# Kernel tuning notes

Hardware: AMD Instinct MI355X
Metric: run time of the kernel (lower is better)

The kernel has to match this reference:

```python
import jax, jax.numpy as jnp
import numpy as np

B, IN, H, OUT = 8192, 1024, 1024, 512


def setup_inputs() -> dict:
    key = jax.random.key(0)
    ks = jax.random.split(key, 13)
    s_in = 1.0 / np.sqrt(IN + H)
    s_h = 1.0 / np.sqrt(H)
    return {
        "x": jax.random.normal(ks[0], (B, IN), jnp.float32),
        "h": jax.random.normal(ks[1], (B, H), jnp.float32),
        "c": jax.random.normal(ks[2], (B, H), jnp.float32),
        "Wi": jax.random.normal(ks[3], (IN + H, H), jnp.float32) * s_in,
        "bi": jax.random.normal(ks[4], (H,), jnp.float32) * s_in,
        "Wf": jax.random.normal(ks[5], (IN + H, H), jnp.float32) * s_in,
        "bf": jax.random.normal(ks[6], (H,), jnp.float32) * s_in,
        "Wo": jax.random.normal(ks[7], (IN + H, H), jnp.float32) * s_in,
        "bo": jax.random.normal(ks[8], (H,), jnp.float32) * s_in,
        "Wc": jax.random.normal(ks[9], (IN + H, H), jnp.float32) * s_in,
        "bc": jax.random.normal(ks[10], (H,), jnp.float32) * s_in,
        "Wy": jax.random.normal(ks[11], (H, OUT), jnp.float32) * s_h,
        "by": jax.random.normal(ks[12], (OUT,), jnp.float32) * s_h,
    }


def reference(x, h, c, Wi, bi, Wf, bf, Wo, bo, Wc, bc, Wy, by):
    # combined: [B, IN+H]
    combined = jnp.concatenate([x, h], axis=1)
    # Fuse the four gate matmuls into one [B, IN+H] x [IN+H, 4H] GEMM.
    W_all = jnp.concatenate([Wi, Wf, Wo, Wc], axis=1)        # [IN+H, 4H]
    b_all = jnp.concatenate([bi, bf, bo, bc], axis=0)        # [4H]
    gates = combined @ W_all + b_all                          # [B, 4H]
    gi, gf, go, gc = jnp.split(gates, 4, axis=1)
    i_t = jax.nn.sigmoid(gi)
    f_t = jax.nn.sigmoid(gf)
    o_t = jax.nn.sigmoid(go)
    c_tilde = jnp.tanh(gc)
    c_new = f_t * c + i_t * c_tilde
    h_new = o_t * jnp.tanh(c_new)
    y_hat = h_new @ Wy + by                                   # [B, OUT]
    return (y_hat, (h_new, c_new))
```

## Files before the change

kernel.cpp:

```cpp
#include <hip/hip_runtime.h>
#include <hip/hip_bf16.h>
#include <stdint.h>

#define B_ 8192
#define IN_ 1024
#define H_ 1024
#define OUT_ 512
#define KC 2048
#define N4 4096

typedef __bf16 bf16_t;
typedef __bf16 bf16x8 __attribute__((ext_vector_type(8)));
typedef float f32x4 __attribute__((ext_vector_type(4)));

__device__ __forceinline__ void gload_lds16(const void* g, void* l) {
  __builtin_amdgcn_global_load_lds(
      (const __attribute__((address_space(1))) uint32_t*)g,
      (__attribute__((address_space(3))) uint32_t*)l, 16, 0, 0);
}

__device__ __forceinline__ float fsigmoid(float x) {
  return __builtin_amdgcn_rcpf(1.0f + __expf(-x));
}
__device__ __forceinline__ float ftanh(float x) {
  return 2.0f * __builtin_amdgcn_rcpf(1.0f + __expf(-2.0f * x)) - 1.0f;
}


__global__ __launch_bounds__(256) void pack_combined(
    const float* __restrict__ x, const float* __restrict__ h,
    bf16_t* __restrict__ out) {
  const int row = blockIdx.x;
  const int j = threadIdx.x * 8;
  const float* src = (j < IN_) ? (x + (size_t)row * IN_ + j)
                               : (h + (size_t)row * H_ + (j - IN_));
  float4 a = ((const float4*)src)[0];
  float4 b = ((const float4*)src)[1];
  bf16x8 v;
  v[0] = (bf16_t)a.x; v[1] = (bf16_t)a.y; v[2] = (bf16_t)a.z; v[3] = (bf16_t)a.w;
  v[4] = (bf16_t)b.x; v[5] = (bf16_t)b.y; v[6] = (bf16_t)b.z; v[7] = (bf16_t)b.w;
  *(bf16x8*)(out + (size_t)row * KC + j) = v;
}

__global__ __launch_bounds__(256) void transpose_pack4(
    const float* __restrict__ Wi, const float* __restrict__ Wf,
    const float* __restrict__ Wo, const float* __restrict__ Wc,
    bf16_t* __restrict__ dst) {
  const int g = blockIdx.z;
  const float* src = (g == 0) ? Wi : (g == 1) ? Wf : (g == 2) ? Wo : Wc;
  __shared__ float tile[64][65];
  const int k0 = blockIdx.y * 64, n0 = blockIdx.x * 64;
  const int t = threadIdx.x;
  const int tr = t >> 4, tc4 = (t & 15) * 4;
#pragma unroll
  for (int r = 0; r < 4; ++r) {
    const int k = tr + r * 16;
    float4 v = *(const float4*)(src + (size_t)(k0 + k) * H_ + n0 + tc4);
    tile[k][tc4] = v.x; tile[k][tc4 + 1] = v.y;
    tile[k][tc4 + 2] = v.z; tile[k][tc4 + 3] = v.w;
  }
  __syncthreads();
  const int nr = t >> 3, kc8 = (t & 7) * 8;
#pragma unroll
  for (int r = 0; r < 2; ++r) {
    const int n = nr + r * 32;
    bf16x8 v;
#pragma unroll
    for (int q = 0; q < 8; ++q) v[q] = (bf16_t)tile[kc8 + q][n];
    *(bf16x8*)(dst + (size_t)((n0 + n) * 4 + g) * KC + k0 + kc8) = v;
  }
}

__global__ __launch_bounds__(256) void transpose_pack(
    const float* __restrict__ src, bf16_t* __restrict__ dst, int K, int N) {
  __shared__ float tile[64][65];
  const int k0 = blockIdx.y * 64, n0 = blockIdx.x * 64;
  const int t = threadIdx.x;
  const int tr = t >> 4, tc4 = (t & 15) * 4;
#pragma unroll
  for (int r = 0; r < 4; ++r) {
    const int k = tr + r * 16;
    float4 v = *(const float4*)(src + (size_t)(k0 + k) * N + n0 + tc4);
    tile[k][tc4] = v.x; tile[k][tc4 + 1] = v.y;
    tile[k][tc4 + 2] = v.z; tile[k][tc4 + 3] = v.w;
  }
  __syncthreads();
  const int nr = t >> 3, kc8 = (t & 7) * 8;
#pragma unroll
  for (int r = 0; r < 2; ++r) {
    const int n = nr + r * 32;
    bf16x8 v;
#pragma unroll
    for (int q = 0; q < 8; ++q) v[q] = (bf16_t)tile[kc8 + q][n];
    *(bf16x8*)(dst + (size_t)(n0 + n) * K + k0 + kc8) = v;
  }
}

__global__ __launch_bounds__(512) void gemm1_8ph(
    const bf16_t* __restrict__ A, const bf16_t* __restrict__ Bt,
    const float* __restrict__ c_in,
    const float* __restrict__ bi, const float* __restrict__ bfg,
    const float* __restrict__ bo, const float* __restrict__ bc,
    float* __restrict__ h_out, float* __restrict__ c_out,
    bf16_t* __restrict__ hb) {
  constexpr int K = KC;
  constexpr int NT = K / 64;
  __shared__ char lds[131072];

  const int tid = threadIdx.x;
  const int lane = tid & 63;
  const int w = tid >> 6;
  const int wr = w >> 2, wc = w & 3;
  const int l15 = lane & 15, l4 = lane >> 4;

  const int wg = blockIdx.x;
  const int swz = (wg & 7) * 64 + (wg >> 3);
  const int bx = swz >> 5;
  const int by = swz & 31;
  const int m0 = by * 256, n0 = bx * 256;

  const int jrow = lane >> 2;
  const int jcol = ((lane & 3) * 16) ^ ((lane >> 5) << 5);
  const char* Asrc = (const char*)A + (size_t)(m0 + w * 16 + jrow) * (K * 2) + jcol;
  const char* Bsrc = (const char*)Bt + (size_t)(n0 + w * 16 + jrow) * (K * 2) + jcol;
  char* ldsA = lds;
  char* ldsB = lds + 32768;
  const int wchunk = w * 2048;

#define STG_A(buf, h, tt) do {                                            \
    gload_lds16(Asrc + (size_t)(h) * 128 * (K * 2) + (size_t)(tt) * 128,  \
                ldsA + (buf) * 65536 + (h) * 16384 + wchunk);             \
    gload_lds16(Asrc + (size_t)(h) * 128 * (K * 2) + (size_t)(tt) * 128 + 64, \
                ldsA + (buf) * 65536 + (h) * 16384 + wchunk + 1024);      \
  } while (0)
#define STG_B(buf, h, tt) do {                                            \
    gload_lds16(Bsrc + (size_t)(h) * 128 * (K * 2) + (size_t)(tt) * 128,  \
                ldsB + (buf) * 65536 + (h) * 16384 + wchunk);             \
    gload_lds16(Bsrc + (size_t)(h) * 128 * (K * 2) + (size_t)(tt) * 128 + 64, \
                ldsB + (buf) * 65536 + (h) * 16384 + wchunk + 1024);      \
  } while (0)

  const int rdoff = l15 * 64 + ((l4 * 16) ^ ((l15 >> 3) << 5));
  const char* ldsArd = lds + wr * 16384 + rdoff;
  const char* ldsBrd = lds + 32768 + (wc >> 1) * 16384 + (wc & 1) * 8192 + rdoff;

  f32x4 acc[8][4] = {};
  bf16x8 falo[4][2], fahi[4][2], fb[4][2];

  STG_B(0, 0, 0); STG_B(0, 1, 0); STG_A(0, 0, 0); STG_A(0, 1, 0);
  asm volatile("s_waitcnt vmcnt(0)" ::: "memory");
  __builtin_amdgcn_s_barrier();

  for (int t = 0; t < NT; ++t) {
    const int buf = t & 1;
    const int nbuf = buf ^ 1;
    const char* ard = ldsArd + buf * 65536;
    const char* brd = ldsBrd + buf * 65536;
    const bool st1 = (t + 1 < NT);

#pragma unroll
    for (int mi = 0; mi < 2; ++mi)
#pragma unroll
      for (int kk = 0; kk < 2; ++kk)
        falo[mi][kk] = *(const bf16x8*)(ard + mi * 2048 + kk * 1024);
#pragma unroll
    for (int ni = 0; ni < 2; ++ni)
#pragma unroll
      for (int kk = 0; kk < 2; ++kk)
        fb[ni][kk] = *(const bf16x8*)(brd + ni * 2048 + kk * 1024);

    if (st1) {
      STG_B(nbuf, 0, t + 1); STG_B(nbuf, 1, t + 1);
      STG_A(nbuf, 0, t + 1); STG_A(nbuf, 1, t + 1);
    }

#pragma unroll
    for (int mi = 2; mi < 4; ++mi)
#pragma unroll
      for (int kk = 0; kk < 2; ++kk)
        falo[mi][kk] = *(const bf16x8*)(ard + mi * 2048 + kk * 1024);
#pragma unroll
    for (int ni = 2; ni < 4; ++ni)
#pragma unroll
      for (int kk = 0; kk < 2; ++kk)
        fb[ni][kk] = *(const bf16x8*)(brd + ni * 2048 + kk * 1024);

#pragma unroll
    for (int mi = 0; mi < 4; ++mi)
#pragma unroll
      for (int kk = 0; kk < 2; ++kk)
        fahi[mi][kk] = *(const bf16x8*)(ard + (mi + 4) * 2048 + kk * 1024);

    __builtin_amdgcn_s_setprio(1);
#pragma unroll
    for (int kk = 0; kk < 2; ++kk)
#pragma unroll
      for (int mi = 0; mi < 2; ++mi)
#pragma unroll
        for (int ni = 0; ni < 2; ++ni)
          acc[mi][ni] = __builtin_amdgcn_mfma_f32_16x16x32_bf16(
              falo[mi][kk], fb[ni][kk], acc[mi][ni], 0, 0, 0);

#pragma unroll
    for (int kk = 0; kk < 2; ++kk) {
#pragma unroll
      for (int mi = 0; mi < 2; ++mi)
#pragma unroll
        for (int ni = 2; ni < 4; ++ni)
          acc[mi][ni] = __builtin_amdgcn_mfma_f32_16x16x32_bf16(
              falo[mi][kk], fb[ni][kk], acc[mi][ni], 0, 0, 0);
#pragma unroll
      for (int mi = 2; mi < 4; ++mi)
#pragma unroll
        for (int ni = 0; ni < 2; ++ni)
          acc[mi][ni] = __builtin_amdgcn_mfma_f32_16x16x32_bf16(
              falo[mi][kk], fb[ni][kk], acc[mi][ni], 0, 0, 0);
    }

#pragma unroll
    for (int kk = 0; kk < 2; ++kk)
#pragma unroll
      for (int mi = 2; mi < 4; ++mi)
#pragma unroll
        for (int ni = 2; ni < 4; ++ni)
          acc[mi][ni] = __builtin_amdgcn_mfma_f32_16x16x32_bf16(
              falo[mi][kk], fb[ni][kk], acc[mi][ni], 0, 0, 0);

#pragma unroll
    for (int kk = 0; kk < 2; ++kk)
#pragma unroll
      for (int mi = 0; mi < 4; ++mi)
#pragma unroll
        for (int ni = 0; ni < 4; ++ni)
          acc[mi + 4][ni] = __builtin_amdgcn_mfma_f32_16x16x32_bf16(
              fahi[mi][kk], fb[ni][kk], acc[mi + 4][ni], 0, 0, 0);
    __builtin_amdgcn_s_setprio(0);

    if (st1) asm volatile("s_waitcnt vmcnt(0)" ::: "memory");
    __builtin_amdgcn_s_barrier();
  }

  const int hc0 = n0 >> 2;
  const int ehc = tid & 63;
  const int err0 = (tid >> 6) * 8;
  const float bI = bi[hc0 + ehc];
  const float bF = bfg[hc0 + ehc];
  const float bO = bo[hc0 + ehc];
  const float bC = bc[hc0 + ehc];

  for (int p = 0; p < 2; ++p) {
    __builtin_amdgcn_s_barrier();
    {
      float* dst = (float*)(lds + wr * 65536);
      const int mib = p * 4;
#pragma unroll
      for (int mi = 0; mi < 4; ++mi)
#pragma unroll
        for (int ni = 0; ni < 4; ++ni) {
          const int col = wc * 64 + ni * 16 + l15;
          const int hc = col >> 2, g = col & 3;
#pragma unroll
          for (int q = 0; q < 4; ++q) {
            const int rr = mi * 16 + l4 * 4 + q;
            dst[rr * 256 + ((hc ^ rr) * 4) + g] = acc[mib + mi][ni][q];
          }
        }
    }
    __builtin_amdgcn_s_barrier();
#pragma unroll
    for (int half = 0; half < 2; ++half) {
      const float* src = (const float*)(lds + half * 65536);
#pragma unroll
      for (int r = 0; r < 8; ++r) {
        const int rr = err0 + r;
        f32x4 gq = *(const f32x4*)&src[rr * 256 + ((ehc ^ rr) * 4)];
        const size_t gidx =
            (size_t)(m0 + half * 128 + p * 64 + rr) * H_ + hc0 + ehc;
        float I = fsigmoid(gq[0] + bI);
        float F = fsigmoid(gq[1] + bF);
        float O = fsigmoid(gq[2] + bO);
        float Ct = ftanh(gq[3] + bC);
        float cn = F * c_in[gidx] + I * Ct;
        float hn = O * ftanh(cn);
        c_out[gidx] = cn;
        h_out[gidx] = hn;
        hb[gidx] = (bf16_t)hn;
      }
    }
  }
#undef STG_A
#undef STG_B
}

__global__ __launch_bounds__(256) void gemm_bt_f32(
    const bf16_t* __restrict__ A, const bf16_t* __restrict__ Bt,
    float* __restrict__ Cout, const float* __restrict__ bias,
    int M, int N, int K) {
  __shared__ bf16_t As[128 * 64];
  __shared__ bf16_t Bs[128 * 64];
  const int tid = threadIdx.x;
  const int lane = tid & 63;
  const int wave = tid >> 6;
  const int m0 = blockIdx.y * 128;
  const int n0 = blockIdx.x * 128;
  const int wr = wave >> 1, wc = wave & 1;
  const int l15 = lane & 15, l4 = lane >> 4;

  f32x4 acc[4][4] = {};

  const int srow = tid >> 3;
  const int skel = (tid & 7) * 8;
  const size_t aBase = (size_t)(m0 + srow) * K + skel;
  const size_t bBase = (size_t)(n0 + srow) * K + skel;
  char* aL = (char*)As + wave * 1024;
  char* bL = (char*)Bs + wave * 1024;

  for (int kt = 0; kt < K; kt += 64) {
    __syncthreads();
#pragma unroll
    for (int i = 0; i < 4; ++i) {
      gload_lds16(A + aBase + (size_t)i * 32 * K + kt, aL + i * 4096);
      gload_lds16(Bt + bBase + (size_t)i * 32 * K + kt, bL + i * 4096);
    }
    __syncthreads();
#pragma unroll
    for (int kk = 0; kk < 2; ++kk) {
      bf16x8 af[4], bq[4];
#pragma unroll
      for (int mi = 0; mi < 4; ++mi)
        af[mi] = *(const bf16x8*)((const char*)As +
                 (wr * 64 + mi * 16 + l15) * 128 + kk * 64 + l4 * 16);
#pragma unroll
      for (int ni = 0; ni < 4; ++ni)
        bq[ni] = *(const bf16x8*)((const char*)Bs +
                 (wc * 64 + ni * 16 + l15) * 128 + kk * 64 + l4 * 16);
#pragma unroll
      for (int mi = 0; mi < 4; ++mi)
#pragma unroll
        for (int ni = 0; ni < 4; ++ni)
          acc[mi][ni] = __builtin_amdgcn_mfma_f32_16x16x32_bf16(
              af[mi], bq[ni], acc[mi][ni], 0, 0, 0);
    }
  }

  const int col = n0 + wc * 64 + l15;
  const int row0 = m0 + wr * 64 + l4 * 4;
#pragma unroll
  for (int ni = 0; ni < 4; ++ni) {
    const float bv = bias[col + ni * 16];
#pragma unroll
    for (int mi = 0; mi < 4; ++mi)
#pragma unroll
      for (int q = 0; q < 4; ++q)
        Cout[(size_t)(row0 + mi * 16 + q) * N + col + ni * 16] =
            acc[mi][ni][q] + bv;
  }
}

extern "C" void kernel_launch(void* const* d_in, const int* in_sizes, int n_in,
                              void* d_out, int out_size, void* d_ws,
                              size_t ws_size, hipStream_t stream) {
  const float* x = (const float*)d_in[0];
  const float* h = (const float*)d_in[1];
  const float* c = (const float*)d_in[2];
  const float* Wi = (const float*)d_in[3];
  const float* bi = (const float*)d_in[4];
  const float* Wf = (const float*)d_in[5];
  const float* bfg = (const float*)d_in[6];
  const float* Wo = (const float*)d_in[7];
  const float* bo = (const float*)d_in[8];
  const float* Wc = (const float*)d_in[9];
  const float* bc = (const float*)d_in[10];
  const float* Wy = (const float*)d_in[11];
  const float* by = (const float*)d_in[12];

  char* ws = (char*)d_ws;
  bf16_t* combined = (bf16_t*)ws;
  bf16_t* Wt = (bf16_t*)(ws + 33554432);
  bf16_t* Wyt = (bf16_t*)(ws + 33554432 + 16777216);
  bf16_t* hb = (bf16_t*)(ws + 33554432 + 16777216 + 1048576);

  float* y_out = (float*)d_out;
  float* h_out = y_out + (size_t)B_ * OUT_;
  float* c_out = h_out + (size_t)B_ * H_;

  pack_combined<<<dim3(B_), dim3(256), 0, stream>>>(x, h, combined);
  transpose_pack4<<<dim3(H_ / 64, KC / 64, 4), dim3(256), 0, stream>>>(
      Wi, Wf, Wo, Wc, Wt);
  transpose_pack<<<dim3(OUT_ / 64, H_ / 64), dim3(256), 0, stream>>>(
      Wy, Wyt, H_, OUT_);

  gemm1_8ph<<<dim3((B_ / 256) * (N4 / 256)), dim3(512), 0, stream>>>(
      combined, Wt, c, bi, bfg, bo, bc, h_out, c_out, hb);

  gemm_bt_f32<<<dim3(OUT_ / 128, B_ / 128), dim3(256), 0, stream>>>(
      hb, Wyt, y_out, by, B_, OUT_, H_);
}
```

Measured before the change: 196.2 us.

## Merge weight transposes, prefetch c_in in epilogue, swizzle LDS in output GEMM

Merges the two weight transpose kernels into one launch, using a z-slice for Wy and early-returning blocks outside its range. Loads the c_in values for the gemm1 epilogue into registers before the LDS staging loop, so their global latency overlaps the barriers. Applies an XOR swizzle to the 16-byte LDS chunks in the second GEMM, on both the global-to-LDS loads and the fragment reads, to reduce LDS bank conflicts. The changes cost extra registers in the epilogue and some idle blocks in the merged transpose launch.

```diff
diff --git a/kernel.cpp b/kernel.cpp
--- a/kernel.cpp
+++ b/kernel.cpp
@@ -42,37 +42,22 @@
   *(bf16x8*)(out + (size_t)row * KC + j) = v;
 }
 
-__global__ __launch_bounds__(256) void transpose_pack4(
+__global__ __launch_bounds__(256) void transpose_all(
     const float* __restrict__ Wi, const float* __restrict__ Wf,
     const float* __restrict__ Wo, const float* __restrict__ Wc,
-    bf16_t* __restrict__ dst) {
-  const int g = blockIdx.z;
-  const float* src = (g == 0) ? Wi : (g == 1) ? Wf : (g == 2) ? Wo : Wc;
-  __shared__ float tile[64][65];
-  const int k0 = blockIdx.y * 64, n0 = blockIdx.x * 64;
-  const int t = threadIdx.x;
-  const int tr = t >> 4, tc4 = (t & 15) * 4;
-#pragma unroll
-  for (int r = 0; r < 4; ++r) {
-    const int k = tr + r * 16;
-    float4 v = *(const float4*)(src + (size_t)(k0 + k) * H_ + n0 + tc4);
-    tile[k][tc4] = v.x; tile[k][tc4 + 1] = v.y;
-    tile[k][tc4 + 2] = v.z; tile[k][tc4 + 3] = v.w;
-  }
-  __syncthreads();
-  const int nr = t >> 3, kc8 = (t & 7) * 8;
-#pragma unroll
-  for (int r = 0; r < 2; ++r) {
-    const int n = nr + r * 32;
-    bf16x8 v;
-#pragma unroll
-    for (int q = 0; q < 8; ++q) v[q] = (bf16_t)tile[kc8 + q][n];
-    *(bf16x8*)(dst + (size_t)((n0 + n) * 4 + g) * KC + k0 + kc8) = v;
-  }
-}
-
-__global__ __launch_bounds__(256) void transpose_pack(
-    const float* __restrict__ src, bf16_t* __restrict__ dst, int K, int N) {
+    const float* __restrict__ Wy, bf16_t* __restrict__ dstG,
+    bf16_t* __restrict__ dstY) {
+  const int z = blockIdx.z;
+  const float* src;
+  bf16_t* dst;
+  int K, N, RS, RO;
+  if (z < 4) {
+    src = (z == 0) ? Wi : (z == 1) ? Wf : (z == 2) ? Wo : Wc;
+    dst = dstG; K = KC; N = H_; RS = 4; RO = z;
+  } else {
+    if (blockIdx.x >= 8 || blockIdx.y >= 16) return;
+    src = Wy; dst = dstY; K = H_; N = OUT_; RS = 1; RO = 0;
+  }
   __shared__ float tile[64][65];
   const int k0 = blockIdx.y * 64, n0 = blockIdx.x * 64;
   const int t = threadIdx.x;
@@ -92,7 +77,7 @@
     bf16x8 v;
 #pragma unroll
     for (int q = 0; q < 8; ++q) v[q] = (bf16_t)tile[kc8 + q][n];
-    *(bf16x8*)(dst + (size_t)(n0 + n) * K + k0 + kc8) = v;
+    *(bf16x8*)(dst + (size_t)((n0 + n) * RS + RO) * K + k0 + kc8) = v;
   }
 }
 
@@ -248,6 +233,16 @@
   const float bO = bo[hc0 + ehc];
   const float bC = bc[hc0 + ehc];
 
+  float cpre[2][2][8];
+#pragma unroll
+  for (int p = 0; p < 2; ++p)
+#pragma unroll
+    for (int half = 0; half < 2; ++half)
+#pragma unroll
+      for (int r = 0; r < 8; ++r)
+        cpre[p][half][r] =
+            c_in[(size_t)(m0 + half * 128 + p * 64 + err0 + r) * H_ + hc0 + ehc];
+
   for (int p = 0; p < 2; ++p) {
     __builtin_amdgcn_s_barrier();
     {
@@ -280,7 +275,7 @@
         float F = fsigmoid(gq[1] + bF);
         float O = fsigmoid(gq[2] + bO);
         float Ct = ftanh(gq[3] + bC);
-        float cn = F * c_in[gidx] + I * Ct;
+        float cn = F * cpre[p][half][r] + I * Ct;
         float hn = O * ftanh(cn);
         c_out[gidx] = cn;
         h_out[gidx] = hn;
@@ -309,18 +304,21 @@
   f32x4 acc[4][4] = {};
 
   const int srow = tid >> 3;
-  const int skel = (tid & 7) * 8;
-  const size_t aBase = (size_t)(m0 + srow) * K + skel;
-  const size_t bBase = (size_t)(n0 + srow) * K + skel;
+  const int slot = tid & 7;
+  const int skelb = (slot * 16) ^ ((srow & 7) << 4);
+  const char* aSrc = (const char*)A + (size_t)(m0 + srow) * (K * 2) + skelb;
+  const char* bSrc = (const char*)Bt + (size_t)(n0 + srow) * (K * 2) + skelb;
   char* aL = (char*)As + wave * 1024;
   char* bL = (char*)Bs + wave * 1024;
 
+  const int xr = (l15 & 7) << 4;
+
   for (int kt = 0; kt < K; kt += 64) {
     __syncthreads();
 #pragma unroll
     for (int i = 0; i < 4; ++i) {
-      gload_lds16(A + aBase + (size_t)i * 32 * K + kt, aL + i * 4096);
-      gload_lds16(Bt + bBase + (size_t)i * 32 * K + kt, bL + i * 4096);
+      gload_lds16(aSrc + ((size_t)i * 32 * K + kt) * 2, aL + i * 4096);
+      gload_lds16(bSrc + ((size_t)i * 32 * K + kt) * 2, bL + i * 4096);
     }
     __syncthreads();
 #pragma unroll
@@ -329,11 +327,11 @@
 #pragma unroll
       for (int mi = 0; mi < 4; ++mi)
         af[mi] = *(const bf16x8*)((const char*)As +
-                 (wr * 64 + mi * 16 + l15) * 128 + kk * 64 + l4 * 16);
+                 (wr * 64 + mi * 16 + l15) * 128 + ((kk * 64 + l4 * 16) ^ xr));
 #pragma unroll
       for (int ni = 0; ni < 4; ++ni)
         bq[ni] = *(const bf16x8*)((const char*)Bs +
-                 (wc * 64 + ni * 16 + l15) * 128 + kk * 64 + l4 * 16);
+                 (wc * 64 + ni * 16 + l15) * 128 + ((kk * 64 + l4 * 16) ^ xr));
 #pragma unroll
       for (int mi = 0; mi < 4; ++mi)
 #pragma unroll
@@ -385,10 +383,8 @@
   float* c_out = h_out + (size_t)B_ * H_;
 
   pack_combined<<<dim3(B_), dim3(256), 0, stream>>>(x, h, combined);
-  transpose_pack4<<<dim3(H_ / 64, KC / 64, 4), dim3(256), 0, stream>>>(
-      Wi, Wf, Wo, Wc, Wt);
-  transpose_pack<<<dim3(OUT_ / 64, H_ / 64), dim3(256), 0, stream>>>(
-      Wy, Wyt, H_, OUT_);
+  transpose_all<<<dim3(16, 32, 5), dim3(256), 0, stream>>>(
+      Wi, Wf, Wo, Wc, Wy, Wt, Wyt);
 
   gemm1_8ph<<<dim3((B_ / 256) * (N4 / 256)), dim3(512), 0, stream>>>(
       combined, Wt, c, bi, bfg, bo, bc, h_out, c_out, hb);
```

Result: faster. 185.6 us, median of 2 (-5.4%).
